# Kernel tuning notes

Hardware: AMD Instinct MI355X
Metric: run time of the kernel (lower is better)

## Reference

```python
import jax, jax.numpy as jnp
import numpy as np

NUG = 1e-6  # diagonal nugget for numerical stability


def covmat(x1, x2, lmb):
    """Product Matern-3/2 kernel with per-dim log-lengthscales lmb[:-1] and log-scale lmb[-1].
    k(x,x') = exp(lmb[-1]) * prod_j (1+|dx_j|/l_j) * exp(-|dx_j|/l_j).
    Loops over the small fixed input dim d to avoid an [n1,n2,d] intermediate."""
    ls = jnp.exp(lmb[:-1])
    x1s = x1 / ls  # [n1, d]
    x2s = x2 / ls  # [n2, d]
    d = x1.shape[1]
    C0 = jnp.ones((x1.shape[0], x2.shape[0]), x1.dtype)
    V = jnp.zeros((x1.shape[0], x2.shape[0]), x1.dtype)
    for j in range(d):
        S = jnp.abs(x1s[:, j][:, None] - x2s[:, j][None, :])
        C0 = C0 * (1.0 + S)
        V = V - S
    return jnp.exp(lmb[-1]) * C0 * jnp.exp(V)


def cov_sp(theta, thetai, lmb):
    """Inducing-point (Nystrom/FITC) covariance decomposition.
    C = Delta + U U^T with U = c_fi Ci^{-1/2}; returns Delta^{-1} diag, Q_half with
    C^{-1} = Delta^{-1} - Q_half Q_half^T, and logdet(C)."""
    p = thetai.shape[0]
    c_fi = covmat(theta, thetai, lmb)                      # [n, p]
    C_i = covmat(thetai, thetai, lmb)
    C_i = C_i + NUG * jnp.exp(lmb[-1]) * jnp.eye(p, dtype=theta.dtype)
    W_Ci, U_Ci = jnp.linalg.eigh(C_i)
    Ciinvh = U_Ci / jnp.sqrt(W_Ci)                         # Ci^{-1/2}
    Crh = c_fi @ Ciinvh                                    # [n, p]
    diagC = jnp.exp(lmb[-1]) * (1.0 + NUG)                 # k(x,x)
    Delta_diag = jnp.maximum(diagC - jnp.sum(Crh * Crh, axis=1), NUG)
    Delta_inv_diag = 1.0 / Delta_diag                      # [n]
    R = jnp.eye(p, dtype=theta.dtype) + Crh.T @ (Delta_inv_diag[:, None] * Crh)
    W_R, U_R = jnp.linalg.eigh(R)
    Q_half = (Delta_inv_diag[:, None] * Crh) @ (U_R / jnp.sqrt(W_R)) @ U_R.T  # [n, p]
    logdet_C = jnp.sum(jnp.log(Delta_diag)) + jnp.sum(jnp.log(W_R))
    return Delta_inv_diag, Q_half, logdet_C


def pred_gp_sp(lmb, theta, thetai, thetanew, g):
    """Sparse-GP predictive mean for one latent component: c(new,old) @ C^{-1} g."""
    Delta_inv_diag, Q_half, _ = cov_sp(theta, thetai, lmb)
    Cinv_g = Delta_inv_diag * g - Q_half @ (Q_half.T @ g)  # [n]
    c_new = covmat(thetanew, theta, lmb)                   # [n0, n]
    return c_new @ Cinv_g                                  # [n0]


def setup_inputs() -> dict:
    key = jax.random.key(0)
    ks = jax.random.split(key, 9)
    m, n, p, d, kap, n0 = 12000, 4000, 200, 8, 16, 1000
    theta = jax.random.uniform(ks[0], (n, d), dtype=jnp.float32)
    thetai = jax.random.uniform(ks[1], (p, d), dtype=jnp.float32)
    theta0 = jax.random.uniform(ks[2], (n0, d), dtype=jnp.float32)
    Lmb = jax.random.uniform(ks[3], (kap, d + 1), dtype=jnp.float32, minval=-0.5, maxval=0.5)
    lsigma2 = jax.random.normal(ks[4], (1,), dtype=jnp.float32) - 3.0
    Phi = jax.random.normal(ks[5], (m, kap), dtype=jnp.float32) / np.sqrt(m)
    M = 0.5 * jax.random.normal(ks[6], (kap, n), dtype=jnp.float32)
    Fmean = jax.random.normal(ks[7], (m, 1), dtype=jnp.float32)
    Fstd = jax.random.uniform(ks[8], (m, 1), dtype=jnp.float32, minval=0.5, maxval=1.5)
    return {"theta0": theta0, "Lmb": Lmb, "lsigma2": lsigma2, "Phi": Phi,
            "theta": theta, "thetai": thetai, "M": M, "Fmean": Fmean, "Fstd": Fstd}


def reference(theta0, Lmb, lsigma2, Phi, theta, thetai, M, Fmean, Fstd):
    # vmap the per-latent-component sparse GP prediction over kap (replaces torch loop)
    ghat = jax.vmap(lambda lmb_k, g_k: pred_gp_sp(lmb_k, theta, thetai, theta0, g_k))(Lmb, M)  # [kap, n0]
    fhat = Phi @ ghat                 # [m, n0]
    fhat = fhat * Fstd + Fmean        # un-standardize
    return fhat
```

## Files before the change

kernel.cpp:

```cpp
#include <hip/hip_runtime.h>

#define NN   4000
#define PP   200
#define DD   8
#define KAP  16
#define NN0  1000
#define MMR  12000
#define NUGF 1e-6f

#define RST  204
#define ACST 64
#define PTS   208
#define NTILE 1275

#define OFF_THS    0
#define OFF_THI    (OFF_THS   + KAP*NN*DD)
#define OFF_TH0S   (OFF_THI   + KAP*PP*DD)
#define OFF_AFULL  (OFF_TH0S  + KAP*NN0*DD)
#define OFF_LT     (OFF_AFULL + KAP*PP*PP)
#define OFF_LROW   (OFF_LT    + KAP*PP*PP)
#define OFF_XB     (OFF_LROW  + KAP*PP*PP)
#define OFF_DLI    (OFF_XB    + KAP*PP*PP)
#define OFF_CRH    (OFF_DLI   + KAP*PP)
#define OFF_DINV   (OFF_CRH   + KAP*NN*PP)
#define OFF_DG     (OFF_DINV  + KAP*NN)
#define OFF_VV     (OFF_DG    + KAP*NN)
#define OFF_WV     (OFF_VV    + KAP*PP)
#define OFF_CG     (OFF_WV    + KAP*PP)
#define OFF_GPART  (OFF_CG    + KAP*NN)
#define OFF_GHAT   (OFF_GPART + KAP*4*1024)
#define OFF_RPART  (OFF_GHAT  + KAP*NN0)

__global__ void scale_kernel(const float* __restrict__ theta, const float* __restrict__ thetai,
                             const float* __restrict__ theta0, const float* __restrict__ Lmb,
                             float* __restrict__ ths, float* __restrict__ thi, float* __restrict__ th0s) {
  int k = blockIdx.y;
  int idx = blockIdx.x * 256 + threadIdx.x;
  const int total = (NN + PP + NN0) * DD;
  if (idx >= total) return;
  int row = idx >> 3, j = idx & 7;
  float ils = __expf(-Lmb[k * 9 + j]);
  if (row < NN) {
    ths[(k * NN + row) * DD + j] = theta[row * DD + j] * ils;
  } else if (row < NN + PP) {
    int r = row - NN;
    thi[(k * PP + r) * DD + j] = thetai[r * DD + j] * ils;
  } else {
    int r = row - NN - PP;
    th0s[(k * NN0 + r) * DD + j] = theta0[r * DD + j] * ils;
  }
}

__global__ void buildci_kernel(const float* __restrict__ thi, const float* __restrict__ Lmb,
                               float* __restrict__ A) {
  int k = blockIdx.x;
  __shared__ float ti[PP * DD];
  for (int i = threadIdx.x; i < PP * DD; i += 256) ti[i] = thi[k * PP * DD + i];
  __syncthreads();
  float lsig = Lmb[k * 9 + 8];
  float* Ak = A + k * PP * PP;
  for (int idx = threadIdx.x; idx < PP * PP; idx += 256) {
    int i = idx / PP, j = idx - i * PP;
    float prod = 1.f, sum = 0.f;
#pragma unroll
    for (int t = 0; t < DD; ++t) {
      float s = fabsf(ti[i * DD + t] - ti[j * DD + t]);
      prod = __fmaf_rn(prod, s, prod);
      sum += s;
    }
    float val = prod * __expf(lsig - sum);
    if (i == j) val += NUGF * __expf(lsig);
    Ak[idx] = val;
  }
}

__device__ __forceinline__ float rdlane(float v, int l) {
  return __int_as_float(__builtin_amdgcn_readlane(__float_as_int(v), l));
}

__global__ __launch_bounds__(1024, 4) void chol_kernel(const float* __restrict__ Ain,
                                                       float* __restrict__ LT,
                                                       float* __restrict__ dli) {
  int k = blockIdx.x;
  Ain += (size_t)k * PP * PP; LT += (size_t)k * PP * PP; dli += (size_t)k * PP;
  __shared__ __align__(16) float Ppre[8 * PTS];
  __shared__ __align__(16) float Pt[8 * PTS];
  const int tid = threadIdx.x;

  int t_rt[2], t_ct[2];
  bool t_ok[2];
  float4 acc[2][4];
#pragma unroll
  for (int t = 0; t < 2; ++t) {
    int ti = (tid - 64) + t * 960;
    t_ok[t] = (tid >= 64) && (ti < NTILE);
    int tie = t_ok[t] ? ti : 0;
    int rt = (int)((sqrtf(8.0f * (float)tie + 1.0f) - 1.0f) * 0.5f);
    while ((rt + 1) * (rt + 2) / 2 <= tie) ++rt;
    while (rt * (rt + 1) / 2 > tie) --rt;
    int ct = tie - rt * (rt + 1) / 2;
    t_rt[t] = rt; t_ct[t] = ct;
    if (t_ok[t]) {
      const float* src = Ain + (size_t)(4 * rt) * PP + 4 * ct;
#pragma unroll
      for (int i = 0; i < 4; ++i) acc[t][i] = *(const float4*)(src + (size_t)i * PP);
    } else {
#pragma unroll
      for (int i = 0; i < 4; ++i) acc[t][i] = make_float4(0.f, 0.f, 0.f, 0.f);
    }
  }

  float preg[4][8];
  for (int s = 0; s < 25; ++s) {
    const int jb = 8 * s;
#pragma unroll
    for (int t = 0; t < 2; ++t) {
      if (t_ok[t] && (t_ct[t] >> 1) == s) {
        int q0 = 4 * t_ct[t] - jb;
        int r0 = 4 * t_rt[t];
#pragma unroll
        for (int i = 0; i < 4; ++i) {
          Ppre[(q0 + 0) * PTS + r0 + i] = acc[t][i].x;
          Ppre[(q0 + 1) * PTS + r0 + i] = acc[t][i].y;
          Ppre[(q0 + 2) * PTS + r0 + i] = acc[t][i].z;
          Ppre[(q0 + 3) * PTS + r0 + i] = acc[t][i].w;
        }
      }
    }
    __syncthreads();
    const int nrows = PP - jb;
    if (tid < 64) {
      const int L = tid;
#pragma unroll
      for (int u = 0; u < 4; ++u) {
        int rl = L + 64 * u;
#pragma unroll
        for (int c = 0; c < 8; ++c)
          preg[u][c] = (rl < nrows && rl >= c) ? Ppre[c * PTS + jb + rl] : 0.f;
      }
#pragma unroll
      for (int jj = 0; jj < 8; ++jj) {
        float dv = rdlane(preg[0][jj], jj);
        float l = sqrtf(fmaxf(dv, 1e-12f));
        float inv = 1.0f / l;
#pragma unroll
        for (int u = 0; u < 4; ++u)
          if (u > 0 || L > jj) preg[u][jj] *= inv;
        if (L == jj) { preg[0][jj] = l; dli[jb + jj] = inv; }
#pragma unroll
        for (int c = 0; c < 8; ++c) {
          if (c > jj) {
            float pc = rdlane(preg[0][jj], c);
#pragma unroll
            for (int u = 0; u < 4; ++u)
              preg[u][c] = __fmaf_rn(-preg[u][jj], pc, preg[u][c]);
          }
        }
      }
#pragma unroll
      for (int u = 0; u < 4; ++u) {
        int rl = L + 64 * u;
        if (rl < nrows) {
#pragma unroll
          for (int c = 0; c < 8; ++c) Pt[c * PTS + jb + rl] = preg[u][c];
        }
      }
    }
    __syncthreads();
    if (tid < 64) {
      const int L = tid;
#pragma unroll
      for (int u = 0; u < 4; ++u) {
        int rl = L + 64 * u;
        if (rl < nrows) {
#pragma unroll
          for (int c = 0; c < 8; ++c)
            if (rl >= c) LT[(jb + c) * PP + jb + rl] = preg[u][c];
        }
      }
    }
    const int ctmin = 2 * s + 2;
#pragma unroll
    for (int t = 0; t < 2; ++t) {
      if (t_ok[t] && t_ct[t] >= ctmin) {
        const float* pr = Pt + 4 * t_rt[t];
        const float* pcl = Pt + 4 * t_ct[t];
#pragma unroll
        for (int q = 0; q < 8; ++q) {
          float4 a = *(const float4*)(pr + q * PTS);
          float4 b = *(const float4*)(pcl + q * PTS);
          acc[t][0].x = __fmaf_rn(-a.x, b.x, acc[t][0].x);
          acc[t][0].y = __fmaf_rn(-a.x, b.y, acc[t][0].y);
          acc[t][0].z = __fmaf_rn(-a.x, b.z, acc[t][0].z);
          acc[t][0].w = __fmaf_rn(-a.x, b.w, acc[t][0].w);
          acc[t][1].x = __fmaf_rn(-a.y, b.x, acc[t][1].x);
          acc[t][1].y = __fmaf_rn(-a.y, b.y, acc[t][1].y);
          acc[t][1].z = __fmaf_rn(-a.y, b.z, acc[t][1].z);
          acc[t][1].w = __fmaf_rn(-a.y, b.w, acc[t][1].w);
          acc[t][2].x = __fmaf_rn(-a.z, b.x, acc[t][2].x);
          acc[t][2].y = __fmaf_rn(-a.z, b.y, acc[t][2].y);
          acc[t][2].z = __fmaf_rn(-a.z, b.z, acc[t][2].z);
          acc[t][2].w = __fmaf_rn(-a.z, b.w, acc[t][2].w);
          acc[t][3].x = __fmaf_rn(-a.w, b.x, acc[t][3].x);
          acc[t][3].y = __fmaf_rn(-a.w, b.y, acc[t][3].y);
          acc[t][3].z = __fmaf_rn(-a.w, b.z, acc[t][3].z);
          acc[t][3].w = __fmaf_rn(-a.w, b.w, acc[t][3].w);
        }
      }
    }
  }
}

__global__ __launch_bounds__(256) void linv_kernel(const float* __restrict__ LT,
                                                   const float* __restrict__ dli_g,
                                                   float* __restrict__ X) {
  int cb = blockIdx.x, k = blockIdx.y;
  LT += (size_t)k * PP * PP; dli_g += k * PP; X += (size_t)k * PP * PP;
  __shared__ float acc[PP * ACST];
  __shared__ float Pn[8 * PP];
  __shared__ float xf[8 * ACST];
  __shared__ float dl[PP];
  const int tid = threadIdx.x;
  const int i = tid & 63, rg = tid >> 6;
  const int c = cb + 4 * i;
  for (int idx = tid; idx < PP * ACST; idx += 256) acc[idx] = 0.f;
  for (int r = tid; r < PP; r += 256) dl[r] = dli_g[r];
  __syncthreads();
  for (int s = 0; s < 25; ++s) {
    const int t0 = 8 * s;
    for (int idx = tid; idx < 8 * PP; idx += 256) Pn[idx] = LT[t0 * PP + idx];
    __syncthreads();
    if (rg == 0) {
      float xq[8];
#pragma unroll
      for (int q = 0; q < 8; ++q) {
        int t = t0 + q;
        float sv = acc[t * ACST + i];
#pragma unroll
        for (int m = 0; m < 8; ++m)
          if (m < q) sv = __fmaf_rn(Pn[m * PP + t], xq[m], sv);
        float xv = (((t == c) ? 1.0f : 0.0f) - sv) * dl[t];
        xq[q] = xv;
        xf[q * ACST + i] = xv;
        if (c < PP) X[t * PP + c] = xv;
      }
    }
    __syncthreads();
    for (int r = t0 + 8 + rg; r < PP; r += 4) {
      float v = acc[r * ACST + i];
#pragma unroll
      for (int q = 0; q < 8; ++q)
        v = __fmaf_rn(Pn[q * PP + r], xf[q * ACST + i], v);
      acc[r * ACST + i] = v;
    }
    __syncthreads();
  }
}

__global__ __launch_bounds__(256) void rsolve_kernel(const float* __restrict__ X,
                                                     const float* __restrict__ v,
                                                     float* __restrict__ w) {
  int k = blockIdx.x;
  X += (size_t)k * PP * PP; v += k * PP; w += k * PP;
  __shared__ float vl[PP], yl[PP];
  int tid = threadIdx.x, lane = tid & 63, rg = tid >> 6;
  for (int i = tid; i < PP; i += 256) vl[i] = v[i];
  __syncthreads();
  for (int r = rg; r < PP; r += 4) {
    float s = 0.f;
    for (int c = lane; c < PP; c += 64) s = __fmaf_rn(X[r * PP + c], vl[c], s);
#pragma unroll
    for (int off = 32; off > 0; off >>= 1) s += __shfl_xor(s, off, 64);
    if (lane == 0) yl[r] = s;
  }
  __syncthreads();
  if (tid < PP) {
    float s = 0.f;
    for (int r = 0; r < PP; ++r) s = __fmaf_rn(X[r * PP + tid], yl[r], s);
    w[tid] = s;
  }
}

__global__ __launch_bounds__(256) void crh_kernel(const float* __restrict__ ths,
                                                  const float* __restrict__ thi,
                                                  const float* __restrict__ Lmb,
                                                  const float* __restrict__ X,
                                                  const float* __restrict__ Mg,
                                                  float* __restrict__ Crh,
                                                  float* __restrict__ Dinv,
                                                  float* __restrict__ Dg) {
  int k = blockIdx.y, rt = blockIdx.x, r0 = rt * 64;
  const float* thk = ths + k * NN * DD;
  const float* tik = thi + k * PP * DD;
  const float* Xk = X + k * PP * PP;
  float* Ck = Crh + k * NN * PP;
  __shared__ __align__(16) float ts[64 * 9];
  __shared__ __align__(16) float At[16 * 64];
  __shared__ __align__(16) float Bt[16 * 260];
  int tid = threadIdx.x, tx = tid & 15, ty = tid >> 4;
  float lsig = Lmb[k * 9 + 8];
  for (int idx = tid; idx < 64 * DD; idx += 256) {
    int r = idx >> 3, j = idx & 7;
    int rr = r0 + r; if (rr > NN - 1) rr = NN - 1;
    ts[r * 9 + j] = thk[rr * DD + j];
  }
  float acc[4][16];
#pragma unroll
  for (int i = 0; i < 4; ++i)
#pragma unroll
    for (int q = 0; q < 16; ++q) acc[i][q] = 0.f;

  for (int jb = 0; jb < PP; jb += 16) {
    int kc = (PP - jb) < 16 ? (PP - jb) : 16;
    __syncthreads();
    for (int idx = tid; idx < 16 * 256; idx += 256) {
      int kk = idx & 15, i = idx >> 4;
      float vb = 0.f;
      if (kk < kc && i < PP) vb = Xk[i * PP + jb + kk];
      Bt[kk * 260 + i] = vb;
    }
    for (int idx = tid; idx < 16 * 64; idx += 256) {
      int r = idx & 63, kk = idx >> 6;
      float va = 0.f;
      int kkg = jb + kk;
      if (kkg < PP) {
        float prod = 1.f, sum = 0.f;
#pragma unroll
        for (int t = 0; t < DD; ++t) {
          float s = fabsf(ts[r * 9 + t] - tik[kkg * DD + t]);
          prod = __fmaf_rn(prod, s, prod);
          sum += s;
        }
        va = prod * __expf(lsig - sum);
      }
      At[kk * 64 + r] = va;
    }
    __syncthreads();
#pragma unroll
    for (int kk = 0; kk < 16; ++kk) {
      float4 a4 = *(const float4*)&At[kk * 64 + ty * 4];
      const float* bp = &Bt[kk * 260 + tx * 4];
      float bv[16];
      *(float4*)&bv[0]  = *(const float4*)(bp);
      *(float4*)&bv[4]  = *(const float4*)(bp + 64);
      *(float4*)&bv[8]  = *(const float4*)(bp + 128);
      *(float4*)&bv[12] = *(const float4*)(bp + 192);
      float av[4] = {a4.x, a4.y, a4.z, a4.w};
#pragma unroll
      for (int i = 0; i < 4; ++i)
#pragma unroll
        for (int q = 0; q < 16; ++q)
          acc[i][q] = __fmaf_rn(av[i], bv[q], acc[i][q]);
    }
  }
#pragma unroll
  for (int i = 0; i < 4; ++i) {
    int r = r0 + ty * 4 + i;
    if (r < NN) {
#pragma unroll
      for (int q = 0; q < 4; ++q) {
        int c = tx * 4 + 64 * q;
        if (c < PP) {
          float4 v = make_float4(acc[i][q * 4], acc[i][q * 4 + 1], acc[i][q * 4 + 2], acc[i][q * 4 + 3]);
          *(float4*)&Ck[r * PP + c] = v;
        }
      }
    }
  }
  float ss[4];
#pragma unroll
  for (int i = 0; i < 4; ++i) {
    float s = 0.f;
#pragma unroll
    for (int q = 0; q < 16; ++q) s = __fmaf_rn(acc[i][q], acc[i][q], s);
    ss[i] = s;
  }
#pragma unroll
  for (int off = 1; off <= 8; off <<= 1) {
#pragma unroll
    for (int i = 0; i < 4; ++i) ss[i] += __shfl_xor(ss[i], off);
  }
  if (tx == 0) {
    float sig = __expf(lsig);
#pragma unroll
    for (int i = 0; i < 4; ++i) {
      int r = r0 + ty * 4 + i;
      if (r < NN) {
        float delta = fmaxf(sig * (1.f + NUGF) - ss[i], NUGF);
        float di = 1.f / delta;
        Dinv[k * NN + r] = di;
        Dg[k * NN + r] = di * Mg[(size_t)k * NN + r];
      }
    }
  }
}

template <int NCH>
__global__ __launch_bounds__(256) void syrk_kernel(const float* __restrict__ Crh,
                                                   const float* __restrict__ Dinv,
                                                   const float* __restrict__ M,
                                                   float* __restrict__ Rp) {
  const int CH = NN / NCH;
  int k = blockIdx.z, kch = blockIdx.y;
  int it = blockIdx.x >> 1, jc = blockIdx.x & 1;
  int i0 = it * 64, cb = jc * 128;
  const float* Ck = Crh + (size_t)k * NN * PP;
  float* Rk = Rp + (size_t)(k * NCH + kch) * PP * RST;
  __shared__ __align__(16) float Sc[16 * 64];
  __shared__ __align__(16) float Rw[16 * 128];
  int tid = threadIdx.x, tx = tid & 15, ty = tid >> 4;
  const int kk = ty;
  const int ii4 = tx * 4;
  int rbase0 = kch * CH;
  const float* pA = Ck + (size_t)(rbase0 + kk) * PP + i0 + ii4;
  const float* pB = Ck + (size_t)(rbase0 + kk) * PP + cb + ii4;
  const float* pD = Dinv + (size_t)k * NN + rbase0 + kk;
  const float* pM = M + (size_t)k * NN + rbase0 + kk;
  const bool aok = (i0 + ii4 + 3 < PP);
  const int cg0 = cb + ii4, cg1 = cb + ii4 + 64;
  const bool b0f = (cg0 + 3 < PP);
  const bool b1f = (cg1 + 3 < PP);
  float4 ra, rv0, rv1;
  float acc[4][8];
#pragma unroll
  for (int i = 0; i < 4; ++i)
#pragma unroll
    for (int q = 0; q < 8; ++q) acc[i][q] = 0.f;

  auto stage = [&](int rb) {
    bool rok = (rb + kk < CH);
    float d = rok ? *pD : 0.f;
    if (rok && aok) {
      float4 t = *(const float4*)pA;
      ra = make_float4(t.x * d, t.y * d, t.z * d, t.w * d);
    } else ra = make_float4(0.f, 0.f, 0.f, 0.f);
    if (rok) {
      rv0 = b0f ? *(const float4*)pB : make_float4(0.f, 0.f, 0.f, 0.f);
      if (b1f) rv1 = *(const float4*)(pB + 64);
      else {
        float e[4];
#pragma unroll
        for (int u = 0; u < 4; ++u) {
          int cg = cg1 + u;
          e[u] = (cg < PP) ? pB[64 + u] : ((cg == PP) ? *pM : 0.f);
        }
        rv1 = make_float4(e[0], e[1], e[2], e[3]);
      }
    } else { rv0 = make_float4(0.f, 0.f, 0.f, 0.f); rv1 = rv0; }
    pA += 16 * PP; pB += 16 * PP; pD += 16; pM += 16;
  };
  stage(0);
  for (int rb = 0; rb < CH; rb += 16) {
    __syncthreads();
    *(float4*)&Sc[kk * 64 + ii4] = ra;
    *(float4*)&Rw[kk * 128 + ii4] = rv0;
    *(float4*)&Rw[kk * 128 + ii4 + 64] = rv1;
    __syncthreads();
    stage(rb + 16);
#pragma unroll
    for (int kq = 0; kq < 16; ++kq) {
      float4 a4 = *(const float4*)&Sc[kq * 64 + ty * 4];
      const float* bp = &Rw[kq * 128 + tx * 4];
      float bv[8];
      *(float4*)&bv[0] = *(const float4*)(bp);
      *(float4*)&bv[4] = *(const float4*)(bp + 64);
      float av[4] = {a4.x, a4.y, a4.z, a4.w};
#pragma unroll
      for (int i = 0; i < 4; ++i)
#pragma unroll
        for (int q = 0; q < 8; ++q)
          acc[i][q] = __fmaf_rn(av[i], bv[q], acc[i][q]);
    }
  }
#pragma unroll
  for (int i = 0; i < 4; ++i) {
    int r = i0 + ty * 4 + i;
    if (r < PP) {
#pragma unroll
      for (int q = 0; q < 2; ++q) {
        int c = cb + tx * 4 + 64 * q;
        if (c + 3 < PP) {
          float4 v = make_float4(acc[i][q * 4], acc[i][q * 4 + 1], acc[i][q * 4 + 2], acc[i][q * 4 + 3]);
          *(float4*)&Rk[r * RST + c] = v;
        } else if (c == PP) {
          Rk[r * RST + c] = acc[i][q * 4];
        }
      }
    }
  }
}

template <int NCH>
__global__ void reducer_kernel(const float* __restrict__ Rp, float* __restrict__ A,
                               float* __restrict__ Vv) {
  int k = blockIdx.y;
  int idx = blockIdx.x * 256 + threadIdx.x;
  if (idx < PP * PP) {
    int i = idx / PP, j = idx - i * PP;
    float s = (i == j) ? 1.0f : 0.0f;
    for (int ch = 0; ch < NCH; ++ch) s += Rp[(size_t)((k * NCH + ch) * PP + i) * RST + j];
    A[k * PP * PP + idx] = s;
  }
  if (idx < PP) {
    float sv = 0.f;
    for (int ch = 0; ch < NCH; ++ch) sv += Rp[(size_t)((k * NCH + ch) * PP + idx) * RST + PP];
    Vv[k * PP + idx] = sv;
  }
}

__global__ void cg_kernel(const float* __restrict__ Crh, const float* __restrict__ w,
                          const float* __restrict__ Dinv, const float* __restrict__ Dg,
                          float* __restrict__ Cg) {
  int k = blockIdx.y;
  __shared__ float ws[PP];
  for (int i = threadIdx.x; i < PP; i += 256) ws[i] = w[k * PP + i];
  __syncthreads();
  int r = blockIdx.x * 4 + (threadIdx.x >> 6);
  int lane = threadIdx.x & 63;
  const float* row = Crh + (size_t)(k * NN + r) * PP;
  float s = 0.f;
  for (int c = lane; c < PP; c += 64) s = __fmaf_rn(row[c], ws[c], s);
#pragma unroll
  for (int off = 32; off > 0; off >>= 1) s += __shfl_xor(s, off, 64);
  if (lane == 0) Cg[k * NN + r] = Dg[k * NN + r] - Dinv[k * NN + r] * s;
}

__global__ __launch_bounds__(256) void pred_kernel(const float* __restrict__ th0s,
                                                   const float* __restrict__ ths,
                                                   const float* __restrict__ Lmb,
                                                   const float* __restrict__ Cg,
                                                   float* __restrict__ Gp) {
  int k = blockIdx.z, rch = blockIdx.y, it = blockIdx.x;
  int i0 = it * 256 + threadIdx.x;
  const float* t0k = th0s + k * NN0 * DD;
  const float* thk = ths + k * NN * DD;
  const float* cgk = Cg + k * NN;
  __shared__ float tsl[64 * DD];
  __shared__ float cs[64];
  float t0r[DD];
  int i0c = (i0 < NN0) ? i0 : (NN0 - 1);
#pragma unroll
  for (int j = 0; j < DD; ++j) t0r[j] = t0k[i0c * DD + j];
  float lsig = Lmb[k * 9 + 8];
  float acc = 0.f;
  int rb0 = rch * 1000;
  for (int rb = 0; rb < 1000; rb += 64) {
    __syncthreads();
    for (int idx = threadIdx.x; idx < 64 * DD; idx += 256) {
      int a = rb0 + rb + (idx >> 3);
      if (a > NN - 1) a = NN - 1;
      tsl[idx] = thk[a * DD + (idx & 7)];
    }
    if (threadIdx.x < 64) {
      int rr = rb + threadIdx.x;
      cs[threadIdx.x] = (rr < 1000) ? cgk[rb0 + rr] : 0.f;
    }
    __syncthreads();
#pragma unroll 4
    for (int rr = 0; rr < 64; ++rr) {
      float prod = 1.f, sum = 0.f;
#pragma unroll
      for (int j = 0; j < DD; ++j) {
        float s = fabsf(t0r[j] - tsl[rr * DD + j]);
        prod = __fmaf_rn(prod, s, prod);
        sum += s;
      }
      acc = __fmaf_rn(prod * __expf(lsig - sum), cs[rr], acc);
    }
  }
  if (i0 < NN0) Gp[(k * 4 + rch) * 1024 + i0] = acc;
}

__global__ void gred_kernel(const float* __restrict__ Gp, float* __restrict__ ghat) {
  int idx = blockIdx.x * 256 + threadIdx.x;
  if (idx >= KAP * NN0) return;
  int k = idx / NN0, i0 = idx - k * NN0;
  float s = 0.f;
  for (int ch = 0; ch < 4; ++ch) s += Gp[(k * 4 + ch) * 1024 + i0];
  ghat[idx] = s;
}

__global__ __launch_bounds__(256) void final_kernel(const float* __restrict__ Phi,
                                                    const float* __restrict__ ghat,
                                                    const float* __restrict__ Fmean,
                                                    const float* __restrict__ Fstd,
                                                    float* __restrict__ out) {
  int it = blockIdx.y, jt = blockIdx.x;
  int i0 = it * 64, j = jt * 256 + threadIdx.x;
  __shared__ float ph[64 * KAP];
  __shared__ float fm[64], fs[64];
  for (int idx = threadIdx.x; idx < 64 * KAP; idx += 256) {
    int i = idx >> 4, kk = idx & 15;
    int ii = i0 + i; if (ii > MMR - 1) ii = MMR - 1;
    ph[idx] = Phi[ii * KAP + kk];
  }
  if (threadIdx.x < 64) {
    int ii = i0 + threadIdx.x; if (ii > MMR - 1) ii = MMR - 1;
    fm[threadIdx.x] = Fmean[ii];
    fs[threadIdx.x] = Fstd[ii];
  }
  float gj[KAP];
#pragma unroll
  for (int kk = 0; kk < KAP; ++kk) gj[kk] = (j < NN0) ? ghat[kk * NN0 + j] : 0.f;
  __syncthreads();
  if (j < NN0) {
    for (int i = 0; i < 64; ++i) {
      int ii = i0 + i;
      if (ii >= MMR) break;
      float s = 0.f;
#pragma unroll
      for (int kk = 0; kk < KAP; ++kk) s = __fmaf_rn(ph[i * KAP + kk], gj[kk], s);
      out[(size_t)ii * NN0 + j] = __fmaf_rn(s, fs[i], fm[i]);
    }
  }
}

extern "C" void kernel_launch(void* const* d_in, const int* in_sizes, int n_in,
                              void* d_out, int out_size, void* d_ws, size_t ws_size,
                              hipStream_t stream) {
  const float* theta0 = (const float*)d_in[0];
  const float* Lmb    = (const float*)d_in[1];
  const float* Phi    = (const float*)d_in[3];
  const float* theta  = (const float*)d_in[4];
  const float* thetai = (const float*)d_in[5];
  const float* M      = (const float*)d_in[6];
  const float* Fmean  = (const float*)d_in[7];
  const float* Fstd   = (const float*)d_in[8];
  float* out = (float*)d_out;
  float* ws = (float*)d_ws;

  float* ths   = ws + OFF_THS;
  float* thi   = ws + OFF_THI;
  float* th0s  = ws + OFF_TH0S;
  float* Afull = ws + OFF_AFULL;
  float* LT    = ws + OFF_LT;
  float* Xb    = ws + OFF_XB;
  float* dli   = ws + OFF_DLI;
  float* Crh   = ws + OFF_CRH;
  float* Dinv  = ws + OFF_DINV;
  float* Dg    = ws + OFF_DG;
  float* Vv    = ws + OFF_VV;
  float* Wv    = ws + OFF_WV;
  float* Cg    = ws + OFF_CG;
  float* Gpart = ws + OFF_GPART;
  float* ghat  = ws + OFF_GHAT;
  float* Rpart = ws + OFF_RPART;

  size_t need8 = ((size_t)OFF_RPART + (size_t)KAP * 8 * PP * RST) * sizeof(float);
  int nch = (ws_size >= need8) ? 8 : 4;

  scale_kernel<<<dim3(163, KAP), 256, 0, stream>>>(theta, thetai, theta0, Lmb, ths, thi, th0s);
  buildci_kernel<<<KAP, 256, 0, stream>>>(thi, Lmb, Afull);
  chol_kernel<<<KAP, 1024, 0, stream>>>(Afull, LT, dli);
  linv_kernel<<<dim3(4, KAP), 256, 0, stream>>>(LT, dli, Xb);
  crh_kernel<<<dim3(63, KAP), 256, 0, stream>>>(ths, thi, Lmb, Xb, M, Crh, Dinv, Dg);
  if (nch == 8) {
    syrk_kernel<8><<<dim3(8, 8, KAP), 256, 0, stream>>>(Crh, Dinv, M, Rpart);
    reducer_kernel<8><<<dim3(157, KAP), 256, 0, stream>>>(Rpart, Afull, Vv);
  } else {
    syrk_kernel<4><<<dim3(8, 4, KAP), 256, 0, stream>>>(Crh, Dinv, M, Rpart);
    reducer_kernel<4><<<dim3(157, KAP), 256, 0, stream>>>(Rpart, Afull, Vv);
  }
  chol_kernel<<<KAP, 1024, 0, stream>>>(Afull, LT, dli);
  linv_kernel<<<dim3(4, KAP), 256, 0, stream>>>(LT, dli, Xb);
  rsolve_kernel<<<KAP, 256, 0, stream>>>(Xb, Vv, Wv);
  cg_kernel<<<dim3(1000, KAP), 256, 0, stream>>>(Crh, Wv, Dinv, Dg, Cg);
  pred_kernel<<<dim3(4, 4, KAP), 256, 0, stream>>>(th0s, ths, Lmb, Cg, Gpart);
  gred_kernel<<<63, 256, 0, stream>>>(Gpart, ghat);
  final_kernel<<<dim3(4, 188), 256, 0, stream>>>(Phi, ghat, Fmean, Fstd, out);
}
```

Before: 855.4 us.

## Store inverse Cholesky transposed, prefetch crh B tiles, split pred into more chunks

```diff
diff --git a/kernel.cpp b/kernel.cpp
--- a/kernel.cpp
+++ b/kernel.cpp
@@ -12,6 +12,7 @@
 #define ACST 64
 #define PTS   208
 #define NTILE 1275
+#define BTS  260
 
 #define OFF_THS    0
 #define OFF_THI    (OFF_THS   + KAP*NN*DD)
@@ -28,7 +29,7 @@
 #define OFF_WV     (OFF_VV    + KAP*PP)
 #define OFF_CG     (OFF_WV    + KAP*PP)
 #define OFF_GPART  (OFF_CG    + KAP*NN)
-#define OFF_GHAT   (OFF_GPART + KAP*4*1024)
+#define OFF_GHAT   (OFF_GPART + KAP*8*1024)
 #define OFF_RPART  (OFF_GHAT  + KAP*NN0)
 
 __global__ void scale_kernel(const float* __restrict__ theta, const float* __restrict__ thetai,
@@ -213,9 +214,9 @@
 
 __global__ __launch_bounds__(256) void linv_kernel(const float* __restrict__ LT,
                                                    const float* __restrict__ dli_g,
-                                                   float* __restrict__ X) {
+                                                   float* __restrict__ XT) {
   int cb = blockIdx.x, k = blockIdx.y;
-  LT += (size_t)k * PP * PP; dli_g += k * PP; X += (size_t)k * PP * PP;
+  LT += (size_t)k * PP * PP; dli_g += k * PP; XT += (size_t)k * PP * PP;
   __shared__ float acc[PP * ACST];
   __shared__ float Pn[8 * PP];
   __shared__ float xf[8 * ACST];
@@ -242,10 +243,18 @@
         float xv = (((t == c) ? 1.0f : 0.0f) - sv) * dl[t];
         xq[q] = xv;
         xf[q * ACST + i] = xv;
-        if (c < PP) X[t * PP + c] = xv;
-      }
-    }
-    __syncthreads();
+      }
+    }
+    __syncthreads();
+    if (tid < 128) {
+      int q4 = tid >> 6, il = tid & 63;
+      int c2 = cb + 4 * il;
+      if (c2 < PP) {
+        float4 v4 = make_float4(xf[(q4 * 4 + 0) * ACST + il], xf[(q4 * 4 + 1) * ACST + il],
+                                xf[(q4 * 4 + 2) * ACST + il], xf[(q4 * 4 + 3) * ACST + il]);
+        *(float4*)&XT[(size_t)c2 * PP + t0 + 4 * q4] = v4;
+      }
+    }
     for (int r = t0 + 8 + rg; r < PP; r += 4) {
       float v = acc[r * ACST + i];
 #pragma unroll
@@ -257,18 +266,18 @@
   }
 }
 
-__global__ __launch_bounds__(256) void rsolve_kernel(const float* __restrict__ X,
+__global__ __launch_bounds__(256) void rsolve_kernel(const float* __restrict__ XT,
                                                      const float* __restrict__ v,
                                                      float* __restrict__ w) {
   int k = blockIdx.x;
-  X += (size_t)k * PP * PP; v += k * PP; w += k * PP;
+  XT += (size_t)k * PP * PP; v += k * PP; w += k * PP;
   __shared__ float vl[PP], yl[PP];
   int tid = threadIdx.x, lane = tid & 63, rg = tid >> 6;
   for (int i = tid; i < PP; i += 256) vl[i] = v[i];
   __syncthreads();
   for (int r = rg; r < PP; r += 4) {
     float s = 0.f;
-    for (int c = lane; c < PP; c += 64) s = __fmaf_rn(X[r * PP + c], vl[c], s);
+    for (int c = lane; c < PP; c += 64) s = __fmaf_rn(XT[(size_t)c * PP + r], vl[c], s);
 #pragma unroll
     for (int off = 32; off > 0; off >>= 1) s += __shfl_xor(s, off, 64);
     if (lane == 0) yl[r] = s;
@@ -276,81 +285,114 @@
   __syncthreads();
   if (tid < PP) {
     float s = 0.f;
-    for (int r = 0; r < PP; ++r) s = __fmaf_rn(X[r * PP + tid], yl[r], s);
+    for (int r = 0; r < PP; ++r) s = __fmaf_rn(XT[(size_t)tid * PP + r], yl[r], s);
     w[tid] = s;
   }
 }
 
-__global__ __launch_bounds__(256) void crh_kernel(const float* __restrict__ ths,
-                                                  const float* __restrict__ thi,
-                                                  const float* __restrict__ Lmb,
-                                                  const float* __restrict__ X,
-                                                  const float* __restrict__ Mg,
-                                                  float* __restrict__ Crh,
-                                                  float* __restrict__ Dinv,
-                                                  float* __restrict__ Dg) {
+__global__ __launch_bounds__(256, 4) void crh_kernel(const float* __restrict__ ths,
+                                                     const float* __restrict__ thi,
+                                                     const float* __restrict__ Lmb,
+                                                     const float* __restrict__ XT,
+                                                     const float* __restrict__ Mg,
+                                                     float* __restrict__ Crh,
+                                                     float* __restrict__ Dinv,
+                                                     float* __restrict__ Dg) {
   int k = blockIdx.y, rt = blockIdx.x, r0 = rt * 64;
   const float* thk = ths + k * NN * DD;
-  const float* tik = thi + k * PP * DD;
-  const float* Xk = X + k * PP * PP;
-  float* Ck = Crh + k * NN * PP;
-  __shared__ __align__(16) float ts[64 * 9];
+  const float* XTk = XT + (size_t)k * PP * PP;
+  float* Ck = Crh + (size_t)k * NN * PP;
+  __shared__ __align__(16) float til[PP * DD];
   __shared__ __align__(16) float At[16 * 64];
-  __shared__ __align__(16) float Bt[16 * 260];
+  __shared__ __align__(16) float Bt[16 * BTS];
   int tid = threadIdx.x, tx = tid & 15, ty = tid >> 4;
+  const int lr = tid & 63;
+  const int wq = tid >> 6;
   float lsig = Lmb[k * 9 + 8];
-  for (int idx = tid; idx < 64 * DD; idx += 256) {
-    int r = idx >> 3, j = idx & 7;
-    int rr = r0 + r; if (rr > NN - 1) rr = NN - 1;
-    ts[r * 9 + j] = thk[rr * DD + j];
-  }
+  for (int idx = tid; idx < PP * DD; idx += 256) til[idx] = thi[k * PP * DD + idx];
+  int rr = r0 + lr; if (rr > NN - 1) rr = NN - 1;
+  float t0r[8];
+  *(float4*)&t0r[0] = *(const float4*)&thk[rr * DD];
+  *(float4*)&t0r[4] = *(const float4*)&thk[rr * DD + 4];
+
   float acc[4][16];
 #pragma unroll
   for (int i = 0; i < 4; ++i)
 #pragma unroll
     for (int q = 0; q < 16; ++q) acc[i][q] = 0.f;
 
+  const bool iok = (lr < 50);
+  float4 rb[4];
+#pragma unroll
+  for (int u = 0; u < 4; ++u) {
+    int row = wq + 4 * u;
+    rb[u] = iok ? *(const float4*)&XTk[(size_t)row * PP + lr * 4]
+                : make_float4(0.f, 0.f, 0.f, 0.f);
+  }
+
   for (int jb = 0; jb < PP; jb += 16) {
-    int kc = (PP - jb) < 16 ? (PP - jb) : 16;
-    __syncthreads();
-    for (int idx = tid; idx < 16 * 256; idx += 256) {
-      int kk = idx & 15, i = idx >> 4;
-      float vb = 0.f;
-      if (kk < kc && i < PP) vb = Xk[i * PP + jb + kk];
-      Bt[kk * 260 + i] = vb;
-    }
-    for (int idx = tid; idx < 16 * 64; idx += 256) {
-      int r = idx & 63, kk = idx >> 6;
+    __syncthreads();
+#pragma unroll
+    for (int u = 0; u < 4; ++u) {
+      int kk = wq + 4 * u;
+      *(float4*)&Bt[kk * BTS + lr * 4] = rb[u];
+      int kkg = jb + kk;
       float va = 0.f;
-      int kkg = jb + kk;
       if (kkg < PP) {
-        float prod = 1.f, sum = 0.f;
-#pragma unroll
-        for (int t = 0; t < DD; ++t) {
-          float s = fabsf(ts[r * 9 + t] - tik[kkg * DD + t]);
-          prod = __fmaf_rn(prod, s, prod);
-          sum += s;
-        }
+        float4 lo = *(const float4*)&til[kkg * 8];
+        float4 hi = *(const float4*)&til[kkg * 8 + 4];
+        float prod = 1.f, sum = 0.f, s;
+        s = fabsf(t0r[0] - lo.x); prod = __fmaf_rn(prod, s, prod); sum += s;
+        s = fabsf(t0r[1] - lo.y); prod = __fmaf_rn(prod, s, prod); sum += s;
+        s = fabsf(t0r[2] - lo.z); prod = __fmaf_rn(prod, s, prod); sum += s;
+        s = fabsf(t0r[3] - lo.w); prod = __fmaf_rn(prod, s, prod); sum += s;
+        s = fabsf(t0r[4] - hi.x); prod = __fmaf_rn(prod, s, prod); sum += s;
+        s = fabsf(t0r[5] - hi.y); prod = __fmaf_rn(prod, s, prod); sum += s;
+        s = fabsf(t0r[6] - hi.z); prod = __fmaf_rn(prod, s, prod); sum += s;
+        s = fabsf(t0r[7] - hi.w); prod = __fmaf_rn(prod, s, prod); sum += s;
         va = prod * __expf(lsig - sum);
       }
-      At[kk * 64 + r] = va;
-    }
-    __syncthreads();
+      At[kk * 64 + lr] = va;
+    }
+    __syncthreads();
+    int jn = jb + 16;
+#pragma unroll
+    for (int u = 0; u < 4; ++u) {
+      int row = jn + wq + 4 * u;
+      rb[u] = (iok && row < PP) ? *(const float4*)&XTk[(size_t)row * PP + lr * 4]
+                                : make_float4(0.f, 0.f, 0.f, 0.f);
+    }
 #pragma unroll
     for (int kk = 0; kk < 16; ++kk) {
       float4 a4 = *(const float4*)&At[kk * 64 + ty * 4];
-      const float* bp = &Bt[kk * 260 + tx * 4];
-      float bv[16];
-      *(float4*)&bv[0]  = *(const float4*)(bp);
-      *(float4*)&bv[4]  = *(const float4*)(bp + 64);
-      *(float4*)&bv[8]  = *(const float4*)(bp + 128);
-      *(float4*)&bv[12] = *(const float4*)(bp + 192);
+      const float* bp = &Bt[kk * BTS + tx * 4];
       float av[4] = {a4.x, a4.y, a4.z, a4.w};
-#pragma unroll
-      for (int i = 0; i < 4; ++i)
-#pragma unroll
-        for (int q = 0; q < 16; ++q)
-          acc[i][q] = __fmaf_rn(av[i], bv[q], acc[i][q]);
+      float4 b0 = *(const float4*)(bp);
+      float4 b1 = *(const float4*)(bp + 64);
+#pragma unroll
+      for (int i = 0; i < 4; ++i) {
+        acc[i][0] = __fmaf_rn(av[i], b0.x, acc[i][0]);
+        acc[i][1] = __fmaf_rn(av[i], b0.y, acc[i][1]);
+        acc[i][2] = __fmaf_rn(av[i], b0.z, acc[i][2]);
+        acc[i][3] = __fmaf_rn(av[i], b0.w, acc[i][3]);
+        acc[i][4] = __fmaf_rn(av[i], b1.x, acc[i][4]);
+        acc[i][5] = __fmaf_rn(av[i], b1.y, acc[i][5]);
+        acc[i][6] = __fmaf_rn(av[i], b1.z, acc[i][6]);
+        acc[i][7] = __fmaf_rn(av[i], b1.w, acc[i][7]);
+      }
+      float4 b2 = *(const float4*)(bp + 128);
+      float4 b3 = *(const float4*)(bp + 192);
+#pragma unroll
+      for (int i = 0; i < 4; ++i) {
+        acc[i][8]  = __fmaf_rn(av[i], b2.x, acc[i][8]);
+        acc[i][9]  = __fmaf_rn(av[i], b2.y, acc[i][9]);
+        acc[i][10] = __fmaf_rn(av[i], b2.z, acc[i][10]);
+        acc[i][11] = __fmaf_rn(av[i], b2.w, acc[i][11]);
+        acc[i][12] = __fmaf_rn(av[i], b3.x, acc[i][12]);
+        acc[i][13] = __fmaf_rn(av[i], b3.y, acc[i][13]);
+        acc[i][14] = __fmaf_rn(av[i], b3.z, acc[i][14]);
+        acc[i][15] = __fmaf_rn(av[i], b3.w, acc[i][15]);
+      }
     }
   }
 #pragma unroll
@@ -543,8 +585,8 @@
   for (int j = 0; j < DD; ++j) t0r[j] = t0k[i0c * DD + j];
   float lsig = Lmb[k * 9 + 8];
   float acc = 0.f;
-  int rb0 = rch * 1000;
-  for (int rb = 0; rb < 1000; rb += 64) {
+  int rb0 = rch * 500;
+  for (int rb = 0; rb < 500; rb += 64) {
     __syncthreads();
     for (int idx = threadIdx.x; idx < 64 * DD; idx += 256) {
       int a = rb0 + rb + (idx >> 3);
@@ -552,8 +594,8 @@
       tsl[idx] = thk[a * DD + (idx & 7)];
     }
     if (threadIdx.x < 64) {
-      int rr = rb + threadIdx.x;
-      cs[threadIdx.x] = (rr < 1000) ? cgk[rb0 + rr] : 0.f;
+      int rrr = rb + threadIdx.x;
+      cs[threadIdx.x] = (rrr < 500) ? cgk[rb0 + rrr] : 0.f;
     }
     __syncthreads();
 #pragma unroll 4
@@ -568,7 +610,7 @@
       acc = __fmaf_rn(prod * __expf(lsig - sum), cs[rr], acc);
     }
   }
-  if (i0 < NN0) Gp[(k * 4 + rch) * 1024 + i0] = acc;
+  if (i0 < NN0) Gp[(k * 8 + rch) * 1024 + i0] = acc;
 }
 
 __global__ void gred_kernel(const float* __restrict__ Gp, float* __restrict__ ghat) {
@@ -576,7 +618,7 @@
   if (idx >= KAP * NN0) return;
   int k = idx / NN0, i0 = idx - k * NN0;
   float s = 0.f;
-  for (int ch = 0; ch < 4; ++ch) s += Gp[(k * 4 + ch) * 1024 + i0];
+  for (int ch = 0; ch < 8; ++ch) s += Gp[(k * 8 + ch) * 1024 + i0];
   ghat[idx] = s;
 }
 
@@ -665,7 +707,7 @@
   linv_kernel<<<dim3(4, KAP), 256, 0, stream>>>(LT, dli, Xb);
   rsolve_kernel<<<KAP, 256, 0, stream>>>(Xb, Vv, Wv);
   cg_kernel<<<dim3(1000, KAP), 256, 0, stream>>>(Crh, Wv, Dinv, Dg, Cg);
-  pred_kernel<<<dim3(4, 4, KAP), 256, 0, stream>>>(th0s, ths, Lmb, Cg, Gpart);
+  pred_kernel<<<dim3(4, 8, KAP), 256, 0, stream>>>(th0s, ths, Lmb, Cg, Gpart);
   gred_kernel<<<63, 256, 0, stream>>>(Gpart, ghat);
   final_kernel<<<dim3(4, 188), 256, 0, stream>>>(Phi, ghat, Fmean, Fstd, out);
 }
```

Result: slower. 984.8 us (+15.1%).

## Store inverse Cholesky factor transposed and split prediction over more row chunks

Applied to the files above, without the earlier changes.

```diff
diff --git a/kernel.cpp b/kernel.cpp
--- a/kernel.cpp
+++ b/kernel.cpp
@@ -12,6 +12,7 @@
 #define ACST 64
 #define PTS   208
 #define NTILE 1275
+#define BTS  260
 
 #define OFF_THS    0
 #define OFF_THI    (OFF_THS   + KAP*NN*DD)
@@ -28,7 +29,7 @@
 #define OFF_WV     (OFF_VV    + KAP*PP)
 #define OFF_CG     (OFF_WV    + KAP*PP)
 #define OFF_GPART  (OFF_CG    + KAP*NN)
-#define OFF_GHAT   (OFF_GPART + KAP*4*1024)
+#define OFF_GHAT   (OFF_GPART + KAP*8*1024)
 #define OFF_RPART  (OFF_GHAT  + KAP*NN0)
 
 __global__ void scale_kernel(const float* __restrict__ theta, const float* __restrict__ thetai,
@@ -213,9 +214,9 @@
 
 __global__ __launch_bounds__(256) void linv_kernel(const float* __restrict__ LT,
                                                    const float* __restrict__ dli_g,
-                                                   float* __restrict__ X) {
+                                                   float* __restrict__ XT) {
   int cb = blockIdx.x, k = blockIdx.y;
-  LT += (size_t)k * PP * PP; dli_g += k * PP; X += (size_t)k * PP * PP;
+  LT += (size_t)k * PP * PP; dli_g += k * PP; XT += (size_t)k * PP * PP;
   __shared__ float acc[PP * ACST];
   __shared__ float Pn[8 * PP];
   __shared__ float xf[8 * ACST];
@@ -242,10 +243,18 @@
         float xv = (((t == c) ? 1.0f : 0.0f) - sv) * dl[t];
         xq[q] = xv;
         xf[q * ACST + i] = xv;
-        if (c < PP) X[t * PP + c] = xv;
-      }
-    }
-    __syncthreads();
+      }
+    }
+    __syncthreads();
+    if (tid < 128) {
+      int q4 = tid >> 6, il = tid & 63;
+      int c2 = cb + 4 * il;
+      if (c2 < PP) {
+        float4 v4 = make_float4(xf[(q4 * 4 + 0) * ACST + il], xf[(q4 * 4 + 1) * ACST + il],
+                                xf[(q4 * 4 + 2) * ACST + il], xf[(q4 * 4 + 3) * ACST + il]);
+        *(float4*)&XT[(size_t)c2 * PP + t0 + 4 * q4] = v4;
+      }
+    }
     for (int r = t0 + 8 + rg; r < PP; r += 4) {
       float v = acc[r * ACST + i];
 #pragma unroll
@@ -257,18 +266,18 @@
   }
 }
 
-__global__ __launch_bounds__(256) void rsolve_kernel(const float* __restrict__ X,
+__global__ __launch_bounds__(256) void rsolve_kernel(const float* __restrict__ XT,
                                                      const float* __restrict__ v,
                                                      float* __restrict__ w) {
   int k = blockIdx.x;
-  X += (size_t)k * PP * PP; v += k * PP; w += k * PP;
+  XT += (size_t)k * PP * PP; v += k * PP; w += k * PP;
   __shared__ float vl[PP], yl[PP];
   int tid = threadIdx.x, lane = tid & 63, rg = tid >> 6;
   for (int i = tid; i < PP; i += 256) vl[i] = v[i];
   __syncthreads();
   for (int r = rg; r < PP; r += 4) {
     float s = 0.f;
-    for (int c = lane; c < PP; c += 64) s = __fmaf_rn(X[r * PP + c], vl[c], s);
+    for (int c = lane; c < PP; c += 64) s = __fmaf_rn(XT[(size_t)c * PP + r], vl[c], s);
 #pragma unroll
     for (int off = 32; off > 0; off >>= 1) s += __shfl_xor(s, off, 64);
     if (lane == 0) yl[r] = s;
@@ -276,7 +285,7 @@
   __syncthreads();
   if (tid < PP) {
     float s = 0.f;
-    for (int r = 0; r < PP; ++r) s = __fmaf_rn(X[r * PP + tid], yl[r], s);
+    for (int r = 0; r < PP; ++r) s = __fmaf_rn(XT[(size_t)tid * PP + r], yl[r], s);
     w[tid] = s;
   }
 }
@@ -284,7 +293,7 @@
 __global__ __launch_bounds__(256) void crh_kernel(const float* __restrict__ ths,
                                                   const float* __restrict__ thi,
                                                   const float* __restrict__ Lmb,
-                                                  const float* __restrict__ X,
+                                                  const float* __restrict__ XT,
                                                   const float* __restrict__ Mg,
                                                   float* __restrict__ Crh,
                                                   float* __restrict__ Dinv,
@@ -292,12 +301,14 @@
   int k = blockIdx.y, rt = blockIdx.x, r0 = rt * 64;
   const float* thk = ths + k * NN * DD;
   const float* tik = thi + k * PP * DD;
-  const float* Xk = X + k * PP * PP;
-  float* Ck = Crh + k * NN * PP;
+  const float* XTk = XT + (size_t)k * PP * PP;
+  float* Ck = Crh + (size_t)k * NN * PP;
   __shared__ __align__(16) float ts[64 * 9];
   __shared__ __align__(16) float At[16 * 64];
-  __shared__ __align__(16) float Bt[16 * 260];
+  __shared__ __align__(16) float Bt[16 * BTS];
   int tid = threadIdx.x, tx = tid & 15, ty = tid >> 4;
+  const int lr = tid & 63;
+  const int wq = tid >> 6;
   float lsig = Lmb[k * 9 + 8];
   for (int idx = tid; idx < 64 * DD; idx += 256) {
     int r = idx >> 3, j = idx & 7;
@@ -310,14 +321,17 @@
 #pragma unroll
     for (int q = 0; q < 16; ++q) acc[i][q] = 0.f;
 
+  const bool iok = (lr < 50);
+
   for (int jb = 0; jb < PP; jb += 16) {
-    int kc = (PP - jb) < 16 ? (PP - jb) : 16;
-    __syncthreads();
-    for (int idx = tid; idx < 16 * 256; idx += 256) {
-      int kk = idx & 15, i = idx >> 4;
-      float vb = 0.f;
-      if (kk < kc && i < PP) vb = Xk[i * PP + jb + kk];
-      Bt[kk * 260 + i] = vb;
+    __syncthreads();
+#pragma unroll
+    for (int u = 0; u < 4; ++u) {
+      int kk = wq + 4 * u;
+      int row = jb + kk;
+      float4 vb = (iok && row < PP) ? *(const float4*)&XTk[(size_t)row * PP + lr * 4]
+                                    : make_float4(0.f, 0.f, 0.f, 0.f);
+      *(float4*)&Bt[kk * BTS + lr * 4] = vb;
     }
     for (int idx = tid; idx < 16 * 64; idx += 256) {
       int r = idx & 63, kk = idx >> 6;
@@ -339,7 +353,7 @@
 #pragma unroll
     for (int kk = 0; kk < 16; ++kk) {
       float4 a4 = *(const float4*)&At[kk * 64 + ty * 4];
-      const float* bp = &Bt[kk * 260 + tx * 4];
+      const float* bp = &Bt[kk * BTS + tx * 4];
       float bv[16];
       *(float4*)&bv[0]  = *(const float4*)(bp);
       *(float4*)&bv[4]  = *(const float4*)(bp + 64);
@@ -543,8 +557,8 @@
   for (int j = 0; j < DD; ++j) t0r[j] = t0k[i0c * DD + j];
   float lsig = Lmb[k * 9 + 8];
   float acc = 0.f;
-  int rb0 = rch * 1000;
-  for (int rb = 0; rb < 1000; rb += 64) {
+  int rb0 = rch * 500;
+  for (int rb = 0; rb < 500; rb += 64) {
     __syncthreads();
     for (int idx = threadIdx.x; idx < 64 * DD; idx += 256) {
       int a = rb0 + rb + (idx >> 3);
@@ -552,8 +566,8 @@
       tsl[idx] = thk[a * DD + (idx & 7)];
     }
     if (threadIdx.x < 64) {
-      int rr = rb + threadIdx.x;
-      cs[threadIdx.x] = (rr < 1000) ? cgk[rb0 + rr] : 0.f;
+      int rrr = rb + threadIdx.x;
+      cs[threadIdx.x] = (rrr < 500) ? cgk[rb0 + rrr] : 0.f;
     }
     __syncthreads();
 #pragma unroll 4
@@ -568,7 +582,7 @@
       acc = __fmaf_rn(prod * __expf(lsig - sum), cs[rr], acc);
     }
   }
-  if (i0 < NN0) Gp[(k * 4 + rch) * 1024 + i0] = acc;
+  if (i0 < NN0) Gp[(k * 8 + rch) * 1024 + i0] = acc;
 }
 
 __global__ void gred_kernel(const float* __restrict__ Gp, float* __restrict__ ghat) {
@@ -576,7 +590,7 @@
   if (idx >= KAP * NN0) return;
   int k = idx / NN0, i0 = idx - k * NN0;
   float s = 0.f;
-  for (int ch = 0; ch < 4; ++ch) s += Gp[(k * 4 + ch) * 1024 + i0];
+  for (int ch = 0; ch < 8; ++ch) s += Gp[(k * 8 + ch) * 1024 + i0];
   ghat[idx] = s;
 }
 
@@ -665,7 +679,7 @@
   linv_kernel<<<dim3(4, KAP), 256, 0, stream>>>(LT, dli, Xb);
   rsolve_kernel<<<KAP, 256, 0, stream>>>(Xb, Vv, Wv);
   cg_kernel<<<dim3(1000, KAP), 256, 0, stream>>>(Crh, Wv, Dinv, Dg, Cg);
-  pred_kernel<<<dim3(4, 4, KAP), 256, 0, stream>>>(th0s, ths, Lmb, Cg, Gpart);
+  pred_kernel<<<dim3(4, 8, KAP), 256, 0, stream>>>(th0s, ths, Lmb, Cg, Gpart);
   gred_kernel<<<63, 256, 0, stream>>>(Gpart, ghat);
   final_kernel<<<dim3(4, 188), 256, 0, stream>>>(Phi, ghat, Fmean, Fstd, out);
 }
```

New measurement: 814.9 us. -4.7%, faster.
